# Optimization experiments

Hardware: AMD Instinct MI355X
Metric: run time of the kernel (lower is better)

The kernel has to match this reference:

```python
import jax, jax.numpy as jnp
import numpy as np

N_NODES = 100000
N_EDGES = 3200000
F_IN = 512
HIDDEN = 16
N_LABELS = 64


def _degree_norms(edge_src, edge_dst, n):
    # DGL GraphConv norm='both': src side uses out-degree, dst side uses in-degree,
    # both clamped to min 1, raised to -1/2.
    ones = jnp.ones(edge_src.shape[0], dtype=jnp.float32)
    deg_out = jax.ops.segment_sum(ones, edge_src, num_segments=n)
    deg_in = jax.ops.segment_sum(ones, edge_dst, num_segments=n)
    norm_src = jax.lax.rsqrt(jnp.maximum(deg_out, 1.0))
    norm_dst = jax.lax.rsqrt(jnp.maximum(deg_in, 1.0))
    return norm_src, norm_dst


def setup_inputs() -> dict:
    key = jax.random.key(0)
    k_x, k_s, k_d, k_w1, k_b1, k_w2, k_b2 = jax.random.split(key, 7)
    features = jax.random.normal(k_x, (N_NODES, F_IN), dtype=jnp.float32)
    edge_src = jax.random.randint(k_s, (N_EDGES,), 0, N_NODES, dtype=jnp.int64)
    edge_dst = jax.random.randint(k_d, (N_EDGES,), 0, N_NODES, dtype=jnp.int64)
    # GraphConv params (glorot-ish scale)
    W1 = jax.random.normal(k_w1, (F_IN, HIDDEN), dtype=jnp.float32) * (1.0 / np.sqrt(F_IN))
    b1 = jnp.zeros((HIDDEN,), dtype=jnp.float32)
    W2 = jax.random.normal(k_w2, (HIDDEN, N_LABELS), dtype=jnp.float32) * (1.0 / np.sqrt(HIDDEN))
    b2 = jnp.zeros((N_LABELS,), dtype=jnp.float32)
    return {"features": features, "W1": W1, "b1": b1, "W2": W2, "b2": b2,
            "edge_src": edge_src, "edge_dst": edge_dst}


def reference(features, W1, b1, W2, b2, edge_src, edge_dst):
    n = features.shape[0]
    norm_src, norm_dst = _degree_norms(edge_src, edge_dst, n)

    # Layer 1: in_feats (512) > out_feats (16) -> DGL projects first, then aggregates.
    h = features * norm_src[:, None]          # [N, 512]
    h = h @ W1                                 # [N, 16]
    h = jax.ops.segment_sum(h[edge_src], edge_dst, num_segments=n)  # SpMM gather+scatter
    h = h * norm_dst[:, None] + b1
    h = jax.nn.relu(h)  # GraphConv activation; outer F.relu is idempotent

    # Layer 2: in_feats (16) <= out_feats (64) -> DGL aggregates first, then projects.
    h2 = h * norm_src[:, None]                 # [N, 16]
    h2 = jax.ops.segment_sum(h2[edge_src], edge_dst, num_segments=n)
    h2 = h2 * norm_dst[:, None]
    out = h2 @ W2 + b2                          # [N, 64]
    return out
```

## Files before the change

kernel.cpp:

```cpp
#include <hip/hip_runtime.h>

#define N_NODES 100000
#define N_EDGES 3200000
#define F_IN 512
#define HIDDEN 16
#define N_LABELS 64

#define BW 128
#define NBUCK ((N_NODES + BW - 1) / BW)
#define NCB 256
#define SCAN_N (NBUCK * NCB)
#define SCAN_BLKS ((SCAN_N + 1023) / 1024)
#define CAP 10240

__global__ __launch_bounds__(256) void count_kernel(
        const int* __restrict__ es, const int* __restrict__ ed,
        int* __restrict__ Msrc, int* __restrict__ Mdst) {
    __shared__ int h1[NBUCK], h2[NBUCK];
    const int tid = threadIdx.x, g = blockIdx.x;
    for (int i = tid; i < NBUCK; i += 256) { h1[i] = 0; h2[i] = 0; }
    __syncthreads();
    for (int i = g * 256 + tid; i < N_EDGES; i += NCB * 256) {
        atomicAdd(&h1[es[i] >> 7], 1);
        atomicAdd(&h2[ed[i] >> 7], 1);
    }
    __syncthreads();
    for (int i = tid; i < NBUCK; i += 256) {
        Msrc[i * NCB + g] = h1[i];
        Mdst[i * NCB + g] = h2[i];
    }
}

__global__ __launch_bounds__(256) void scanA_kernel(int* __restrict__ a, int* __restrict__ bsum) {
    __shared__ int s[256];
    const int tid = threadIdx.x;
    const int base = blockIdx.x * 1024 + tid * 4;
    int4 v = make_int4(0, 0, 0, 0);
    if (base + 3 < SCAN_N) v = *(const int4*)(a + base);
    else {
        if (base + 0 < SCAN_N) v.x = a[base + 0];
        if (base + 1 < SCAN_N) v.y = a[base + 1];
        if (base + 2 < SCAN_N) v.z = a[base + 2];
        if (base + 3 < SCAN_N) v.w = a[base + 3];
    }
    const int lsum = v.x + v.y + v.z + v.w;
    s[tid] = lsum;
    __syncthreads();
    for (int off = 1; off < 256; off <<= 1) {
        int t = (tid >= off) ? s[tid - off] : 0;
        __syncthreads();
        s[tid] += t;
        __syncthreads();
    }
    int e0 = s[tid] - lsum;
    int e1 = e0 + v.x, e2 = e1 + v.y, e3 = e2 + v.z;
    if (base + 3 < SCAN_N) *(int4*)(a + base) = make_int4(e0, e1, e2, e3);
    else {
        if (base + 0 < SCAN_N) a[base + 0] = e0;
        if (base + 1 < SCAN_N) a[base + 1] = e1;
        if (base + 2 < SCAN_N) a[base + 2] = e2;
        if (base + 3 < SCAN_N) a[base + 3] = e3;
    }
    if (tid == 255) bsum[blockIdx.x] = s[255];
}

__global__ void scanB_kernel(int* __restrict__ bsum) {
    __shared__ int s[256];
    const int tid = threadIdx.x;
    int v = (tid < SCAN_BLKS) ? bsum[tid] : 0;
    s[tid] = v;
    __syncthreads();
    for (int off = 1; off < 256; off <<= 1) {
        int t = (tid >= off) ? s[tid - off] : 0;
        __syncthreads();
        s[tid] += t;
        __syncthreads();
    }
    if (tid < SCAN_BLKS) bsum[tid] = s[tid] - v;
}

__global__ __launch_bounds__(256) void scanC_kernel(int* __restrict__ a, const int* __restrict__ bsum) {
    const int base = blockIdx.x * 1024 + threadIdx.x * 4;
    const int b = bsum[blockIdx.x];
    if (base + 3 < SCAN_N) {
        int4 v = *(int4*)(a + base);
        v.x += b; v.y += b; v.z += b; v.w += b;
        *(int4*)(a + base) = v;
    } else {
        for (int j = 0; j < 4; ++j) if (base + j < SCAN_N) a[base + j] += b;
    }
}

__global__ __launch_bounds__(256) void scatter_kernel(
        const int* __restrict__ es, const int* __restrict__ ed,
        const int* __restrict__ Ssrc, const int* __restrict__ Sdst,
        unsigned* __restrict__ pairs, unsigned char* __restrict__ srcb) {
    __shared__ int c1[NBUCK], c2[NBUCK];
    const int tid = threadIdx.x, g = blockIdx.x;
    for (int i = tid; i < NBUCK; i += 256) {
        c1[i] = Ssrc[i * NCB + g];
        c2[i] = Sdst[i * NCB + g];
    }
    __syncthreads();
    for (int i = g * 256 + tid; i < N_EDGES; i += NCB * 256) {
        int s = es[i], d = ed[i];
        int p2 = atomicAdd(&c2[d >> 7], 1);
        pairs[p2] = ((unsigned)(d & 127) << 17) | (unsigned)s;
        int p1 = atomicAdd(&c1[s >> 7], 1);
        srcb[p1] = (unsigned char)(s & 127);
    }
}

__global__ __launch_bounds__(256) void csr_kernel(
        const int* __restrict__ Sdst, unsigned* __restrict__ pairs,
        int* __restrict__ row_ptr, float* __restrict__ norm_dst) {
    __shared__ unsigned buf[CAP];
    __shared__ int hist[BW], scn[BW], cur[BW];
    const int b = blockIdx.x, tid = threadIdx.x;
    const int base  = Sdst[b * NCB];
    const int nextb = (b == NBUCK - 1) ? N_EDGES : Sdst[(b + 1) * NCB];
    const int nb = nextb - base;
    const bool fits = (nb <= CAP);
    if (tid < BW) hist[tid] = 0;
    __syncthreads();
    for (int i = tid; i < nb; i += 256) {
        unsigned pk = pairs[base + i];
        if (fits) buf[i] = pk;
        atomicAdd(&hist[pk >> 17], 1);
    }
    __syncthreads();
    if (tid < BW) scn[tid] = hist[tid];
    __syncthreads();
    for (int off = 1; off < BW; off <<= 1) {
        int t = 0;
        if (tid < BW && tid >= off) t = scn[tid - off];
        __syncthreads();
        if (tid < BW) scn[tid] += t;
        __syncthreads();
    }
    if (tid < BW) {
        int e = scn[tid] - hist[tid];
        cur[tid] = e;
        int node = b * BW + tid;
        if (node <= N_NODES) row_ptr[node] = base + e;
        if (node < N_NODES) norm_dst[node] = rsqrtf(fmaxf((float)hist[tid], 1.0f));
    }
    __syncthreads();
    if (fits) {
        for (int i = tid; i < nb; i += 256) {
            unsigned pk = buf[i];
            int pos = atomicAdd(&cur[pk >> 17], 1);
            pairs[base + pos] = pk & 0x1FFFFu;
        }
    } else {
        for (int i = tid; i < nb; i += 256)
            pairs[base + i] &= 0x1FFFFu;
    }
}

__global__ __launch_bounds__(256) void srcdeg_kernel(
        const int* __restrict__ Ssrc, const unsigned char* __restrict__ srcb,
        float* __restrict__ norm_src) {
    __shared__ int hist[BW];
    const int b = blockIdx.x, tid = threadIdx.x;
    const int base  = Ssrc[b * NCB];
    const int nextb = (b == NBUCK - 1) ? N_EDGES : Ssrc[(b + 1) * NCB];
    const int nb = nextb - base;
    if (tid < BW) hist[tid] = 0;
    __syncthreads();
    for (int i = tid; i < nb; i += 256)
        atomicAdd(&hist[srcb[base + i]], 1);
    __syncthreads();
    if (tid < BW) {
        int node = b * BW + tid;
        if (node < N_NODES) norm_src[node] = rsqrtf(fmaxf((float)hist[tid], 1.0f));
    }
}

#define MM_NODES 256
#define MM_CH 32
#define MM_S 257
#define KSPLIT 2

__global__ __launch_bounds__(256, 4) void proj1_kernel(
        const float* __restrict__ X, const float* __restrict__ W1,
        float* __restrict__ P0, float* __restrict__ P1) {
    __shared__ float xsT[MM_CH][MM_S];
    __shared__ float w1c[MM_CH][HIDDEN];

    const int tid = threadIdx.x;
    const int node0 = blockIdx.x * MM_NODES;
    const int z = blockIdx.y;
    const int g  = tid >> 2;
    const int kq = (tid & 3) * 4;

    float acc[4][4];
#pragma unroll
    for (int a = 0; a < 4; ++a)
#pragma unroll
        for (int b = 0; b < 4; ++b) acc[a][b] = 0.f;

    const int CHUNKS = (F_IN / MM_CH) / KSPLIT;
    for (int cc = 0; cc < CHUNKS; ++cc) {
        const int c = z * CHUNKS + cc;
        __syncthreads();
        if (tid < MM_CH * HIDDEN / 4)
            ((float4*)&w1c[0][0])[tid] = ((const float4*)(W1 + c * MM_CH * HIDDEN))[tid];
#pragma unroll
        for (int it = 0; it < 8; ++it) {
            int i  = tid + it * 256;
            int r  = i >> 3;
            int c4 = i & 7;
            float4 v = make_float4(0.f, 0.f, 0.f, 0.f);
            int gn = node0 + r;
            if (gn < N_NODES)
                v = *((const float4*)(X + (size_t)gn * F_IN + c * MM_CH + c4 * 4));
            int j = c4 * 4;
            xsT[j + 0][r] = v.x;
            xsT[j + 1][r] = v.y;
            xsT[j + 2][r] = v.z;
            xsT[j + 3][r] = v.w;
        }
        __syncthreads();
#pragma unroll
        for (int j = 0; j < MM_CH; ++j) {
            float4 f = *((const float4*)&xsT[j][g * 4]);
            float4 w = *((const float4*)&w1c[j][kq]);
            acc[0][0] += f.x * w.x; acc[0][1] += f.x * w.y; acc[0][2] += f.x * w.z; acc[0][3] += f.x * w.w;
            acc[1][0] += f.y * w.x; acc[1][1] += f.y * w.y; acc[1][2] += f.y * w.z; acc[1][3] += f.y * w.w;
            acc[2][0] += f.z * w.x; acc[2][1] += f.z * w.y; acc[2][2] += f.z * w.z; acc[2][3] += f.z * w.w;
            acc[3][0] += f.w * w.x; acc[3][1] += f.w * w.y; acc[3][2] += f.w * w.z; acc[3][3] += f.w * w.w;
        }
    }

    float* Pz = z ? P1 : P0;
#pragma unroll
    for (int a = 0; a < 4; ++a) {
        int gn = node0 + g * 4 + a;
        if (gn < N_NODES)
            *((float4*)(Pz + (size_t)gn * HIDDEN + kq)) =
                make_float4(acc[a][0], acc[a][1], acc[a][2], acc[a][3]);
    }
}

__global__ void reduce1_kernel(const float* __restrict__ P0, const float* __restrict__ P1,
                               const float* __restrict__ norm_src, float* __restrict__ H1) {
    int gid = blockIdx.x * blockDim.x + threadIdx.x;
    if (gid < N_NODES * 4) {
        float4 a = ((const float4*)P0)[gid];
        float4 b = ((const float4*)P1)[gid];
        float ns = norm_src[gid >> 2];
        ((float4*)H1)[gid] = make_float4((a.x + b.x) * ns, (a.y + b.y) * ns,
                                         (a.z + b.z) * ns, (a.w + b.w) * ns);
    }
}

__global__ __launch_bounds__(256) void spmm1_kernel(
        const int* __restrict__ rp, const int* __restrict__ col,
        const float* __restrict__ H1, const float* __restrict__ norm_dst,
        const float* __restrict__ norm_src, const float* __restrict__ b1,
        float* __restrict__ H1b) {
    int tid = threadIdx.x;
    int node = blockIdx.x * 16 + (tid >> 4);
    int k = tid & 15;
    if (node >= N_NODES) return;
    int beg = rp[node], end = rp[node + 1];
    float acc = 0.f;
    int j = beg;
    for (; j + 3 < end; j += 4) {
        int s0 = col[j], s1 = col[j + 1], s2 = col[j + 2], s3 = col[j + 3];
        float v0 = H1[(size_t)s0 * HIDDEN + k];
        float v1 = H1[(size_t)s1 * HIDDEN + k];
        float v2 = H1[(size_t)s2 * HIDDEN + k];
        float v3 = H1[(size_t)s3 * HIDDEN + k];
        acc += v0 + v1 + v2 + v3;
    }
    for (; j < end; ++j) acc += H1[(size_t)col[j] * HIDDEN + k];
    float v = fmaxf(acc * norm_dst[node] + b1[k], 0.f) * norm_src[node];
    H1b[(size_t)node * HIDDEN + k] = v;
}

__global__ __launch_bounds__(256) void spmm2_final_kernel(
        const int* __restrict__ rp, const int* __restrict__ col,
        const float* __restrict__ H1b, const float* __restrict__ norm_dst,
        const float* __restrict__ W2, const float* __restrict__ b2,
        float* __restrict__ out) {
    __shared__ float w2s[HIDDEN * N_LABELS];
    int tid = threadIdx.x;
    ((float4*)w2s)[tid] = ((const float4*)W2)[tid];
    __syncthreads();

    int node = blockIdx.x * 16 + (tid >> 4);
    int k = tid & 15;
    if (node >= N_NODES) return;
    int beg = rp[node], end = rp[node + 1];
    float acc = 0.f;
    int j = beg;
    for (; j + 3 < end; j += 4) {
        int s0 = col[j], s1 = col[j + 1], s2 = col[j + 2], s3 = col[j + 3];
        float v0 = H1b[(size_t)s0 * HIDDEN + k];
        float v1 = H1b[(size_t)s1 * HIDDEN + k];
        float v2 = H1b[(size_t)s2 * HIDDEN + k];
        float v3 = H1b[(size_t)s3 * HIDDEN + k];
        acc += v0 + v1 + v2 + v3;
    }
    for (; j < end; ++j) acc += H1b[(size_t)col[j] * HIDDEN + k];
    acc *= norm_dst[node];

    float4 o = ((const float4*)b2)[k];
#pragma unroll
    for (int jj = 0; jj < HIDDEN; ++jj) {
        float hj = __shfl(acc, jj, 16);
        float4 w = *((const float4*)&w2s[jj * N_LABELS + 4 * k]);
        o.x += hj * w.x; o.y += hj * w.y; o.z += hj * w.z; o.w += hj * w.w;
    }
    ((float4*)out)[(size_t)node * 16 + k] = o;
}

extern "C" void kernel_launch(void* const* d_in, const int* in_sizes, int n_in,
                              void* d_out, int out_size, void* d_ws, size_t ws_size,
                              hipStream_t stream) {
    const float* X  = (const float*)d_in[0];
    const float* W1 = (const float*)d_in[1];
    const float* b1 = (const float*)d_in[2];
    const float* W2 = (const float*)d_in[3];
    const float* b2 = (const float*)d_in[4];
    const int* es   = (const int*)d_in[5];
    const int* ed   = (const int*)d_in[6];
    float* out = (float*)d_out;

    char* ws = (char*)d_ws;
    float* norm_src = (float*)ws;  ws += (size_t)N_NODES * 4;
    float* norm_dst = (float*)ws;  ws += (size_t)N_NODES * 4;
    int*   row_ptr  = (int*)ws;    ws += 400016;
    char*  R1 = ws;                ws += (size_t)N_NODES * HIDDEN * 4;
    char*  R2 = ws;                ws += (size_t)N_NODES * HIDDEN * 4;
    char*  R3 = ws;

    unsigned char* srcb = (unsigned char*)R1;
    float* P0  = (float*)R1;
    float* H1  = (float*)R1;
    int*   Sdst = (int*)R2;
    int*   Ssrc = (int*)(R2 + 800768);
    int*   bs1  = (int*)(R2 + 1601536);
    int*   bs2  = (int*)(R2 + 1602560);
    float* P1   = (float*)R2;
    float* H1b  = (float*)R2;
    unsigned* pairs = (unsigned*)R3;
    int*   col  = (int*)R3;

    const int NPB = (N_NODES + MM_NODES - 1) / MM_NODES;

    count_kernel<<<NCB, 256, 0, stream>>>(es, ed, Ssrc, Sdst);
    scanA_kernel<<<SCAN_BLKS, 256, 0, stream>>>(Sdst, bs1);
    scanA_kernel<<<SCAN_BLKS, 256, 0, stream>>>(Ssrc, bs2);
    scanB_kernel<<<1, 256, 0, stream>>>(bs1);
    scanB_kernel<<<1, 256, 0, stream>>>(bs2);
    scanC_kernel<<<SCAN_BLKS, 256, 0, stream>>>(Sdst, bs1);
    scanC_kernel<<<SCAN_BLKS, 256, 0, stream>>>(Ssrc, bs2);
    scatter_kernel<<<NCB, 256, 0, stream>>>(es, ed, Ssrc, Sdst, pairs, srcb);
    csr_kernel<<<NBUCK, 256, 0, stream>>>(Sdst, pairs, row_ptr, norm_dst);
    srcdeg_kernel<<<NBUCK, 256, 0, stream>>>(Ssrc, srcb, norm_src);
    proj1_kernel<<<dim3(NPB, KSPLIT), 256, 0, stream>>>(X, W1, P0, P1);
    reduce1_kernel<<<(N_NODES * 4 + 255) / 256, 256, 0, stream>>>(P0, P1, norm_src, H1);
    spmm1_kernel<<<(N_NODES + 15) / 16, 256, 0, stream>>>(row_ptr, col, H1, norm_dst, norm_src, b1, H1b);
    spmm2_final_kernel<<<(N_NODES + 15) / 16, 256, 0, stream>>>(row_ptr, col, H1b, norm_dst, W2, b2, out);
}
```

Baseline: 620.4 us.

## Stream X rows directly from global memory in proj1, dropping the shared-memory transpose

The projection kernel no longer stages feature chunks through a transposed shared-memory tile. Each thread now loads float4 slices of its four rows straight from global memory and keeps all of its half of W1 in shared memory, loaded once per block. This removes the per-chunk barriers and LDS transpose traffic, and the block shrinks to 128 threads covering 128 nodes. In exchange each thread's global loads are strided by a full row (2 KB apart across lanes), which may hurt coalescing and cache efficiency on this bandwidth-bound matrix multiply.

```diff
diff --git a/kernel.cpp b/kernel.cpp
--- a/kernel.cpp
+++ b/kernel.cpp
@@ -177,68 +177,76 @@
     }
 }
 
-#define MM_NODES 256
-#define MM_CH 32
-#define MM_S 257
+#define MM_NODES 128
 #define KSPLIT 2
-
-__global__ __launch_bounds__(256, 4) void proj1_kernel(
+#define KH (F_IN / KSPLIT)
+
+__global__ __launch_bounds__(128, 4) void proj1_kernel(
         const float* __restrict__ X, const float* __restrict__ W1,
         float* __restrict__ P0, float* __restrict__ P1) {
-    __shared__ float xsT[MM_CH][MM_S];
-    __shared__ float w1c[MM_CH][HIDDEN];
+    __shared__ float w1c[KH][HIDDEN];
 
     const int tid = threadIdx.x;
     const int node0 = blockIdx.x * MM_NODES;
     const int z = blockIdx.y;
-    const int g  = tid >> 2;
+
+    for (int i = tid; i < KH * HIDDEN / 4; i += 128)
+        ((float4*)&w1c[0][0])[i] = ((const float4*)(W1 + (size_t)z * KH * HIDDEN))[i];
+    __syncthreads();
+
+    const int rg = tid >> 2;
     const int kq = (tid & 3) * 4;
 
+    const float* xr[4];
+    int gn[4];
+#pragma unroll
+    for (int a = 0; a < 4; ++a) {
+        int r = node0 + rg * 4 + a;
+        gn[a] = r;
+        if (r > N_NODES - 1) r = N_NODES - 1;
+        xr[a] = X + (size_t)r * F_IN + (size_t)z * KH;
+    }
+
     float acc[4][4];
 #pragma unroll
     for (int a = 0; a < 4; ++a)
 #pragma unroll
         for (int b = 0; b < 4; ++b) acc[a][b] = 0.f;
 
-    const int CHUNKS = (F_IN / MM_CH) / KSPLIT;
-    for (int cc = 0; cc < CHUNKS; ++cc) {
-        const int c = z * CHUNKS + cc;
-        __syncthreads();
-        if (tid < MM_CH * HIDDEN / 4)
-            ((float4*)&w1c[0][0])[tid] = ((const float4*)(W1 + c * MM_CH * HIDDEN))[tid];
-#pragma unroll
-        for (int it = 0; it < 8; ++it) {
-            int i  = tid + it * 256;
-            int r  = i >> 3;
-            int c4 = i & 7;
-            float4 v = make_float4(0.f, 0.f, 0.f, 0.f);
-            int gn = node0 + r;
-            if (gn < N_NODES)
-                v = *((const float4*)(X + (size_t)gn * F_IN + c * MM_CH + c4 * 4));
-            int j = c4 * 4;
-            xsT[j + 0][r] = v.x;
-            xsT[j + 1][r] = v.y;
-            xsT[j + 2][r] = v.z;
-            xsT[j + 3][r] = v.w;
+    for (int c = 0; c < KH; c += 4) {
+        float4 xv0 = *((const float4*)(xr[0] + c));
+        float4 xv1 = *((const float4*)(xr[1] + c));
+        float4 xv2 = *((const float4*)(xr[2] + c));
+        float4 xv3 = *((const float4*)(xr[3] + c));
+        float4 w0 = *((const float4*)&w1c[c + 0][kq]);
+        float4 w1 = *((const float4*)&w1c[c + 1][kq]);
+        float4 w2 = *((const float4*)&w1c[c + 2][kq]);
+        float4 w3 = *((const float4*)&w1c[c + 3][kq]);
+
+        float xv[4][4];
+        xv[0][0] = xv0.x; xv[0][1] = xv0.y; xv[0][2] = xv0.z; xv[0][3] = xv0.w;
+        xv[1][0] = xv1.x; xv[1][1] = xv1.y; xv[1][2] = xv1.z; xv[1][3] = xv1.w;
+        xv[2][0] = xv2.x; xv[2][1] = xv2.y; xv[2][2] = xv2.z; xv[2][3] = xv2.w;
+        xv[3][0] = xv3.x; xv[3][1] = xv3.y; xv[3][2] = xv3.z; xv[3][3] = xv3.w;
+
+#pragma unroll
+        for (int a = 0; a < 4; ++a) {
+            acc[a][0] += xv[a][0] * w0.x; acc[a][1] += xv[a][0] * w0.y;
+            acc[a][2] += xv[a][0] * w0.z; acc[a][3] += xv[a][0] * w0.w;
+            acc[a][0] += xv[a][1] * w1.x; acc[a][1] += xv[a][1] * w1.y;
+            acc[a][2] += xv[a][1] * w1.z; acc[a][3] += xv[a][1] * w1.w;
+            acc[a][0] += xv[a][2] * w2.x; acc[a][1] += xv[a][2] * w2.y;
+            acc[a][2] += xv[a][2] * w2.z; acc[a][3] += xv[a][2] * w2.w;
+            acc[a][0] += xv[a][3] * w3.x; acc[a][1] += xv[a][3] * w3.y;
+            acc[a][2] += xv[a][3] * w3.z; acc[a][3] += xv[a][3] * w3.w;
         }
-        __syncthreads();
-#pragma unroll
-        for (int j = 0; j < MM_CH; ++j) {
-            float4 f = *((const float4*)&xsT[j][g * 4]);
-            float4 w = *((const float4*)&w1c[j][kq]);
-            acc[0][0] += f.x * w.x; acc[0][1] += f.x * w.y; acc[0][2] += f.x * w.z; acc[0][3] += f.x * w.w;
-            acc[1][0] += f.y * w.x; acc[1][1] += f.y * w.y; acc[1][2] += f.y * w.z; acc[1][3] += f.y * w.w;
-            acc[2][0] += f.z * w.x; acc[2][1] += f.z * w.y; acc[2][2] += f.z * w.z; acc[2][3] += f.z * w.w;
-            acc[3][0] += f.w * w.x; acc[3][1] += f.w * w.y; acc[3][2] += f.w * w.z; acc[3][3] += f.w * w.w;
-        }
     }
 
     float* Pz = z ? P1 : P0;
 #pragma unroll
     for (int a = 0; a < 4; ++a) {
-        int gn = node0 + g * 4 + a;
-        if (gn < N_NODES)
-            *((float4*)(Pz + (size_t)gn * HIDDEN + kq)) =
+        if (gn[a] < N_NODES)
+            *((float4*)(Pz + (size_t)gn[a] * HIDDEN + kq)) =
                 make_float4(acc[a][0], acc[a][1], acc[a][2], acc[a][3]);
     }
 }
@@ -361,7 +369,7 @@
     scatter_kernel<<<NCB, 256, 0, stream>>>(es, ed, Ssrc, Sdst, pairs, srcb);
     csr_kernel<<<NBUCK, 256, 0, stream>>>(Sdst, pairs, row_ptr, norm_dst);
     srcdeg_kernel<<<NBUCK, 256, 0, stream>>>(Ssrc, srcb, norm_src);
-    proj1_kernel<<<dim3(NPB, KSPLIT), 256, 0, stream>>>(X, W1, P0, P1);
+    proj1_kernel<<<dim3(NPB, KSPLIT), 128, 0, stream>>>(X, W1, P0, P1);
     reduce1_kernel<<<(N_NODES * 4 + 255) / 256, 256, 0, stream>>>(P0, P1, norm_src, H1);
     spmm1_kernel<<<(N_NODES + 15) / 16, 256, 0, stream>>>(row_ptr, col, H1, norm_dst, norm_src, b1, H1b);
     spmm2_final_kernel<<<(N_NODES + 15) / 16, 256, 0, stream>>>(row_ptr, col, H1b, norm_dst, W2, b2, out);
```

After: 600.4 us. 1.03x faster.

## Double-buffer proj1 X tiles via direct global-to-LDS loads with swizzled layout

Applied to the files above, without the earlier changes.

Rewrites the layer-1 projection kernel so X tiles are loaded straight into LDS with global_load_lds in a row-major XOR-swizzled layout and double-buffered across K chunks. The whole half of W1 is preloaded once per block, and the old register-staged transpose is dropped. The aim is to overlap the bandwidth-bound X reads with FMA work and remove the transposed LDS stores. In exchange LDS use rises (two buffers plus 16KB of W1), so occupancy hint drops to 2 blocks. Out-of-range rows are clamped rather than zeroed, which is harmless because those rows are never stored.

```diff
diff --git a/kernel.cpp b/kernel.cpp
--- a/kernel.cpp
+++ b/kernel.cpp
@@ -177,21 +177,50 @@
     }
 }
 
-#define MM_NODES 256
-#define MM_CH 32
-#define MM_S 257
+#define P1_ROWS 256
+#define P1_CH 32
 #define KSPLIT 2
-
-__global__ __launch_bounds__(256, 4) void proj1_kernel(
+#define KH (F_IN / KSPLIT)
+#define P1_CHUNKS (KH / P1_CH)
+#define P1_BLKS ((N_NODES + P1_ROWS - 1) / P1_ROWS)
+
+#define GLD16(gp, lp) __builtin_amdgcn_global_load_lds( \
+    (const __attribute__((address_space(1))) unsigned int*)(gp), \
+    (__attribute__((address_space(3))) unsigned int*)(lp), 16, 0, 0)
+
+__global__ __launch_bounds__(256, 2) void proj1_kernel(
         const float* __restrict__ X, const float* __restrict__ W1,
         float* __restrict__ P0, float* __restrict__ P1) {
-    __shared__ float xsT[MM_CH][MM_S];
-    __shared__ float w1c[MM_CH][HIDDEN];
+    __shared__ float xs[2][P1_ROWS * P1_CH];
+    __shared__ float w1c[KH * HIDDEN];
 
     const int tid = threadIdx.x;
-    const int node0 = blockIdx.x * MM_NODES;
+    const int node0 = blockIdx.x * P1_ROWS;
     const int z = blockIdx.y;
-    const int g  = tid >> 2;
+
+    const int srow0 = tid >> 3;
+    const int scg   = tid & 7;
+    const int wbase = tid & 192;
+
+    for (int i = tid; i < KH * HIDDEN / 4; i += 256)
+        ((float4*)w1c)[i] = ((const float4*)(W1 + (size_t)z * KH * HIDDEN))[i];
+
+    {
+        const float* Xc = X + (size_t)z * KH;
+#pragma unroll
+        for (int it = 0; it < 8; ++it) {
+            int row = srow0 + it * 32;
+            int grow = node0 + row;
+            if (grow > N_NODES - 1) grow = N_NODES - 1;
+            int cg = scg ^ ((row >> 2) & 7);
+            const float* gp = Xc + (size_t)grow * F_IN + cg * 4;
+            float* lp = &xs[0][(size_t)(it * 256 + wbase) * 4];
+            GLD16(gp, lp);
+        }
+    }
+    __syncthreads();
+
+    const int rg = tid >> 2;
     const int kq = (tid & 3) * 4;
 
     float acc[4][4];
@@ -200,43 +229,53 @@
 #pragma unroll
         for (int b = 0; b < 4; ++b) acc[a][b] = 0.f;
 
-    const int CHUNKS = (F_IN / MM_CH) / KSPLIT;
-    for (int cc = 0; cc < CHUNKS; ++cc) {
-        const int c = z * CHUNKS + cc;
-        __syncthreads();
-        if (tid < MM_CH * HIDDEN / 4)
-            ((float4*)&w1c[0][0])[tid] = ((const float4*)(W1 + c * MM_CH * HIDDEN))[tid];
-#pragma unroll
-        for (int it = 0; it < 8; ++it) {
-            int i  = tid + it * 256;
-            int r  = i >> 3;
-            int c4 = i & 7;
-            float4 v = make_float4(0.f, 0.f, 0.f, 0.f);
-            int gn = node0 + r;
-            if (gn < N_NODES)
-                v = *((const float4*)(X + (size_t)gn * F_IN + c * MM_CH + c4 * 4));
-            int j = c4 * 4;
-            xsT[j + 0][r] = v.x;
-            xsT[j + 1][r] = v.y;
-            xsT[j + 2][r] = v.z;
-            xsT[j + 3][r] = v.w;
+    for (int cc = 0; cc < P1_CHUNKS; ++cc) {
+        const int cur = cc & 1;
+
+        if (cc + 1 < P1_CHUNKS) {
+            const float* Xc = X + (size_t)z * KH + (size_t)(cc + 1) * P1_CH;
+#pragma unroll
+            for (int it = 0; it < 8; ++it) {
+                int row = srow0 + it * 32;
+                int grow = node0 + row;
+                if (grow > N_NODES - 1) grow = N_NODES - 1;
+                int cg = scg ^ ((row >> 2) & 7);
+                const float* gp = Xc + (size_t)grow * F_IN + cg * 4;
+                float* lp = &xs[cur ^ 1][(size_t)(it * 256 + wbase) * 4];
+                GLD16(gp, lp);
+            }
         }
-        __syncthreads();
-#pragma unroll
-        for (int j = 0; j < MM_CH; ++j) {
-            float4 f = *((const float4*)&xsT[j][g * 4]);
-            float4 w = *((const float4*)&w1c[j][kq]);
-            acc[0][0] += f.x * w.x; acc[0][1] += f.x * w.y; acc[0][2] += f.x * w.z; acc[0][3] += f.x * w.w;
-            acc[1][0] += f.y * w.x; acc[1][1] += f.y * w.y; acc[1][2] += f.y * w.z; acc[1][3] += f.y * w.w;
-            acc[2][0] += f.z * w.x; acc[2][1] += f.z * w.y; acc[2][2] += f.z * w.z; acc[2][3] += f.z * w.w;
-            acc[3][0] += f.w * w.x; acc[3][1] += f.w * w.y; acc[3][2] += f.w * w.z; acc[3][3] += f.w * w.w;
+
+        const float* xb = &xs[cur][0];
+#pragma unroll
+        for (int kk4 = 0; kk4 < 8; ++kk4) {
+            float4 w0 = *((const float4*)&w1c[(cc * P1_CH + kk4 * 4 + 0) * HIDDEN + kq]);
+            float4 w1 = *((const float4*)&w1c[(cc * P1_CH + kk4 * 4 + 1) * HIDDEN + kq]);
+            float4 w2 = *((const float4*)&w1c[(cc * P1_CH + kk4 * 4 + 2) * HIDDEN + kq]);
+            float4 w3 = *((const float4*)&w1c[(cc * P1_CH + kk4 * 4 + 3) * HIDDEN + kq]);
+#pragma unroll
+            for (int a = 0; a < 4; ++a) {
+                int row = rg * 4 + a;
+                int sw  = (row >> 2) & 7;
+                float4 xv = *((const float4*)&xb[row * P1_CH + ((kk4 ^ sw) * 4)]);
+                acc[a][0] += xv.x * w0.x; acc[a][1] += xv.x * w0.y;
+                acc[a][2] += xv.x * w0.z; acc[a][3] += xv.x * w0.w;
+                acc[a][0] += xv.y * w1.x; acc[a][1] += xv.y * w1.y;
+                acc[a][2] += xv.y * w1.z; acc[a][3] += xv.y * w1.w;
+                acc[a][0] += xv.z * w2.x; acc[a][1] += xv.z * w2.y;
+                acc[a][2] += xv.z * w2.z; acc[a][3] += xv.z * w2.w;
+                acc[a][0] += xv.w * w3.x; acc[a][1] += xv.w * w3.y;
+                acc[a][2] += xv.w * w3.z; acc[a][3] += xv.w * w3.w;
+            }
         }
+
+        __syncthreads();
     }
 
     float* Pz = z ? P1 : P0;
 #pragma unroll
     for (int a = 0; a < 4; ++a) {
-        int gn = node0 + g * 4 + a;
+        int gn = node0 + rg * 4 + a;
         if (gn < N_NODES)
             *((float4*)(Pz + (size_t)gn * HIDDEN + kq)) =
                 make_float4(acc[a][0], acc[a][1], acc[a][2], acc[a][3]);
@@ -349,8 +388,6 @@
     unsigned* pairs = (unsigned*)R3;
     int*   col  = (int*)R3;
 
-    const int NPB = (N_NODES + MM_NODES - 1) / MM_NODES;
-
     count_kernel<<<NCB, 256, 0, stream>>>(es, ed, Ssrc, Sdst);
     scanA_kernel<<<SCAN_BLKS, 256, 0, stream>>>(Sdst, bs1);
     scanA_kernel<<<SCAN_BLKS, 256, 0, stream>>>(Ssrc, bs2);
@@ -361,7 +398,7 @@
     scatter_kernel<<<NCB, 256, 0, stream>>>(es, ed, Ssrc, Sdst, pairs, srcb);
     csr_kernel<<<NBUCK, 256, 0, stream>>>(Sdst, pairs, row_ptr, norm_dst);
     srcdeg_kernel<<<NBUCK, 256, 0, stream>>>(Ssrc, srcb, norm_src);
-    proj1_kernel<<<dim3(NPB, KSPLIT), 256, 0, stream>>>(X, W1, P0, P1);
+    proj1_kernel<<<dim3(P1_BLKS, KSPLIT), 256, 0, stream>>>(X, W1, P0, P1);
     reduce1_kernel<<<(N_NODES * 4 + 255) / 256, 256, 0, stream>>>(P0, P1, norm_src, H1);
     spmm1_kernel<<<(N_NODES + 15) / 16, 256, 0, stream>>>(row_ptr, col, H1, norm_dst, norm_src, b1, H1b);
     spmm2_final_kernel<<<(N_NODES + 15) / 16, 256, 0, stream>>>(row_ptr, col, H1b, norm_dst, W2, b2, out);
```

Result: faster. 598.8 us (-3.5%).
